# Kernel optimization log

Hardware: AMD Instinct MI355X
Metric: run time of the kernel (lower is better)

## Reference

```python
import jax, jax.numpy as jnp
import numpy as np

LAYERS, BLOCKS = 10, 3
NL = LAYERS * BLOCKS
DC, RC, SC, CLASSES, K = 128, 128, 256, 256, 2
SR = 4096  # number of output samples sliced from the end
N, L, EN = 4, 8192, 16


def _conv1x1(x, w):
    # x: [N, Cin, L], w: [Cout, Cin] -> [N, Cout, L]
    return jnp.einsum('ncl,oc->nol', x, w)


def _condition(x, enc):
    # x: [N, C, L], enc: [N, C, En], L % En == 0; tiled periodic add (faithful to the view trick)
    n, c, l = x.shape
    en = enc.shape[2]
    return (x.reshape(n, c, l // en, en) + enc[:, :, None, :]).reshape(n, c, l)


def _dilated_causal_conv(x, w, d):
    # kernel_size=2 causal dilated conv. x: [N, Cin, L], w: [Cout, Cin, 2]
    xs = jnp.pad(x, ((0, 0), (0, 0), (d, 0)))[:, :, :x.shape[2]]  # x delayed by d
    return jnp.einsum('ncl,oc->nol', xs, w[:, :, 0]) + jnp.einsum('ncl,oc->nol', x, w[:, :, 1])


def setup_inputs() -> dict:
    key = jax.random.key(0)
    ks = jax.random.split(key, 12)
    s = 0.05
    return {
        'x': jax.random.normal(ks[0], (N, CLASSES, L), jnp.float32),
        'en': jax.random.normal(ks[1], (N, CLASSES, EN), jnp.float32),
        'start1_w': jax.random.normal(ks[2], (RC, CLASSES), jnp.float32) * s,
        'start2_w': jax.random.normal(ks[3], (SC, RC), jnp.float32) * s,
        'cond_w': jax.random.normal(ks[4], (NL, 2 * DC, CLASSES), jnp.float32) * s,
        'dil_w': jax.random.normal(ks[5], (NL, 2 * DC, RC, K), jnp.float32) * s,
        'res_w': jax.random.normal(ks[6], (NL, RC, DC), jnp.float32) * s,
        'skip_w': jax.random.normal(ks[7], (NL, SC, DC), jnp.float32) * s,
        'end1_w': jax.random.normal(ks[8], (CLASSES, SC), jnp.float32) * s,
        'end1_b': jnp.zeros((CLASSES,), jnp.float32),
        'end2_w': jax.random.normal(ks[9], (CLASSES, CLASSES), jnp.float32) * s,
        'end2_b': jnp.zeros((CLASSES,), jnp.float32),
    }


def reference(x, en, start1_w, start2_w, cond_w, dil_w, res_w, skip_w,
              end1_w, end1_b, end2_w, end2_b):
    l = _conv1x1(x, start1_w)          # [N, RC, L]
    s = _conv1x1(l, start2_w)          # [N, SC, L]
    for i in range(NL):
        dil = 2 ** (i % LAYERS)
        d = _dilated_causal_conv(l, dil_w[i], dil)      # [N, 2*DC, L]
        d = _condition(d, _conv1x1(en, cond_w[i]))
        g = jax.nn.sigmoid(d[:, :DC]) * jnp.tanh(d[:, DC:])  # gated, [N, DC, L]
        l = l + _conv1x1(g, res_w[i])
        s = s + _conv1x1(g, skip_w[i])
    s = jax.nn.relu(s)
    s = _conv1x1(s, end1_w) + end1_b[None, :, None]
    s = _condition(s, _conv1x1(en, end2_w) + end2_b[None, :, None])
    s = jax.nn.relu(s)
    return s[:, :, -SR:]
```

## Files before the change

kernel.cpp:

```cpp
#include <hip/hip_runtime.h>

typedef __bf16 bf16_t;
typedef __bf16 bf16x8 __attribute__((ext_vector_type(8)));
typedef __bf16 bf16x4 __attribute__((ext_vector_type(4)));
typedef float  f32x4  __attribute__((ext_vector_type(4)));
typedef int    i32x4  __attribute__((ext_vector_type(4)));

#define PL 136
#define PX 264

__device__ __forceinline__ f32x4 mfma16(bf16x8 a, bf16x8 b, f32x4 c) {
    return __builtin_amdgcn_mfma_f32_16x16x32_bf16(a, b, c, 0, 0, 0);
}

__device__ __forceinline__ void conv_elem(const float* __restrict__ src,
                                          bf16_t* __restrict__ dst,
                                          int idx, int M, int K) {
    int MK = M * K;
    int lay = idx / MK;
    int r = idx - lay * MK;
    int j = r & 7, lane = (r >> 3) & 63, rest = r >> 9;
    int KB = K >> 5;
    int kb = rest % KB, mt = rest / KB;
    int m = mt * 16 + (lane & 15);
    int k = kb * 32 + ((lane >> 4) << 3) + j;
    dst[idx] = (bf16_t)src[(size_t)lay * MK + m * K + k];
}

__global__ void conv_all(const float* __restrict__ rw, const float* __restrict__ kw,
                         const float* __restrict__ s1w, const float* __restrict__ s2w,
                         const float* __restrict__ e1w, const float* __restrict__ dwt,
                         bf16_t* __restrict__ Ares, bf16_t* __restrict__ Askp,
                         bf16_t* __restrict__ A1, bf16_t* __restrict__ A2,
                         bf16_t* __restrict__ Ae, bf16_t* __restrict__ Adil) {
    int idx = blockIdx.x * 256 + threadIdx.x;
    if (idx < 491520) { conv_elem(rw, Ares, idx, 128, 128); return; }
    idx -= 491520;
    if (idx < 983040) { conv_elem(kw, Askp, idx, 256, 128); return; }
    idx -= 983040;
    if (idx < 32768) { conv_elem(s1w, A1, idx, 128, 256); return; }
    idx -= 32768;
    if (idx < 32768) { conv_elem(s2w, A2, idx, 256, 128); return; }
    idx -= 32768;
    if (idx < 65536) { conv_elem(e1w, Ae, idx, 256, 256); return; }
    idx -= 65536;
    if (idx < 1966080) {
        int lay = idx >> 16, r = idx & 65535;
        int j = r & 7, lane = (r >> 3) & 63, rest = r >> 9;
        int kb = rest & 7, mt = rest >> 3;
        int m = mt * 16 + (lane & 15);
        int k = kb * 32 + ((lane >> 4) << 3) + j;
        float v = (k < 128) ? dwt[(((size_t)lay * 256 + m) * 128 + k) * 2]
                            : dwt[(((size_t)lay * 256 + m) * 128 + (k - 128)) * 2 + 1];
        Adil[(size_t)lay * 65536 + r] = (bf16_t)v;
    }
}

__global__ void cond_kernel(const float* __restrict__ cond_w,
                            const float* __restrict__ end2_w,
                            const float* __restrict__ end2_b,
                            const float* __restrict__ en,
                            float* __restrict__ cond_all,
                            float* __restrict__ cond2) {
    __shared__ f32x4 en_s[1024];
    int bi = blockIdx.x;
    int i = bi >> 2, n = bi & 3, o = threadIdx.x;
    const f32x4* ep = (const f32x4*)(en + (size_t)n * 4096);
    for (int idx = threadIdx.x; idx < 1024; idx += 256) en_s[idx] = ep[idx];
    __syncthreads();
    const float* W = (i < 30) ? cond_w + ((size_t)i * 256 + o) * 256
                              : end2_w + (size_t)o * 256;
    f32x4 a0 = {0.f,0.f,0.f,0.f}, a1 = a0, a2 = a0, a3 = a0;
    for (int c = 0; c < 256; c += 4) {
        f32x4 wv = *(const f32x4*)(W + c);
        #pragma unroll
        for (int cc = 0; cc < 4; ++cc) {
            float wf = wv[cc];
            a0 += wf * en_s[(c + cc) * 4 + 0];
            a1 += wf * en_s[(c + cc) * 4 + 1];
            a2 += wf * en_s[(c + cc) * 4 + 2];
            a3 += wf * en_s[(c + cc) * 4 + 3];
        }
    }
    float bias = (i < 30) ? 0.f : end2_b[o];
    float* dst = (i < 30) ? cond_all + (((size_t)i * 4 + n) * 256 + o) * 16
                          : cond2 + ((size_t)n * 256 + o) * 16;
    f32x4* d4 = (f32x4*)dst;
    d4[0] = a0 + bias; d4[1] = a1 + bias; d4[2] = a2 + bias; d4[3] = a3 + bias;
}

__global__ __launch_bounds__(512, 4) void k_start(
    const float* __restrict__ x, bf16_t* __restrict__ la, float* __restrict__ sbuf,
    const bf16_t* __restrict__ A1, const bf16_t* __restrict__ A2, int t_base)
{
    __shared__ __align__(16) bf16_t xt[64 * PX];
    __shared__ __align__(16) bf16_t l0[64 * PL];
    int tid = threadIdx.x;
    int n = blockIdx.y, t0 = t_base + blockIdx.x * 64;
    int lane = tid & 63, w = tid >> 6, i16 = lane & 15, q = lane >> 4;
    f32x4 z = {0.f,0.f,0.f,0.f};
    {
        int t = tid & 63;
        for (int c = tid >> 6; c < 256; c += 8)
            xt[t * PX + c] = (bf16_t)x[((size_t)n * 256 + c) * 8192 + t0 + t];
    }
    __syncthreads();
    f32x4 acc[4] = {z,z,z,z};
    #pragma unroll
    for (int kb = 0; kb < 8; ++kb) {
        int koff = kb * 32 + q * 8;
        bf16x8 bf[4];
        #pragma unroll
        for (int nt = 0; nt < 4; ++nt)
            bf[nt] = *(const bf16x8*)(xt + (nt * 16 + i16) * PX + koff);
        bf16x8 af = *(const bf16x8*)(A1 + (((size_t)w * 8 + kb) * 64 + lane) * 8);
        #pragma unroll
        for (int nt = 0; nt < 4; ++nt) acc[nt] = mfma16(af, bf[nt], acc[nt]);
    }
    #pragma unroll
    for (int nt = 0; nt < 4; ++nt)
        #pragma unroll
        for (int j = 0; j < 4; ++j)
            l0[(nt * 16 + i16) * PL + w * 16 + q * 4 + j] = (bf16_t)acc[nt][j];
    __syncthreads();
    {
        int r = tid >> 4, col = (tid & 15) * 8;
        #pragma unroll
        for (int p = 0; p < 2; ++p) {
            int rr = r + p * 32;
            *(i32x4*)(la + ((size_t)n * 8192 + t0 + rr) * 128 + col) =
                *(const i32x4*)(l0 + rr * PL + col);
        }
    }
    if (t0 >= 4096) {
        f32x4 a2[2][4] = {{z,z,z,z},{z,z,z,z}};
        #pragma unroll
        for (int kb = 0; kb < 4; ++kb) {
            int koff = kb * 32 + q * 8;
            bf16x8 bf[4];
            #pragma unroll
            for (int nt = 0; nt < 4; ++nt)
                bf[nt] = *(const bf16x8*)(l0 + (nt * 16 + i16) * PL + koff);
            #pragma unroll
            for (int mt2 = 0; mt2 < 2; ++mt2) {
                bf16x8 af = *(const bf16x8*)(A2 + ((((size_t)2 * w + mt2) * 4 + kb) * 64 + lane) * 8);
                #pragma unroll
                for (int nt = 0; nt < 4; ++nt) a2[mt2][nt] = mfma16(af, bf[nt], a2[mt2][nt]);
            }
        }
        float* sp = sbuf + (size_t)n * 256 * 4096 + (t0 - 4096);
        #pragma unroll
        for (int mt2 = 0; mt2 < 2; ++mt2)
            #pragma unroll
            for (int nt = 0; nt < 4; ++nt)
                #pragma unroll
                for (int j = 0; j < 4; ++j) {
                    int o = (2 * w + mt2) * 16 + q * 4 + j;
                    sp[(size_t)o * 4096 + nt * 16 + i16] = a2[mt2][nt][j];
                }
    }
}

template<int USEG>
__global__ __launch_bounds__(512, 8) void k_layer(
    const bf16_t* __restrict__ l_in, bf16_t* __restrict__ l_out,
    float* __restrict__ sbuf, bf16_t* __restrict__ Gl,
    const bf16_t* __restrict__ Ad, const bf16_t* __restrict__ Ar,
    const bf16_t* __restrict__ Ak, const float* __restrict__ condL,
    int dil, int t_base, int do_res)
{
    __shared__ __align__(16) bf16_t sm0[32 * PL];
    __shared__ __align__(16) bf16_t sm1[32 * PL];
    __shared__ __align__(16) bf16_t sm2[32 * PL];
    int tid = threadIdx.x;
    int n = blockIdx.y, t0 = t_base + blockIdx.x * 32;
    int lane = tid & 63, w = tid >> 6, i16 = lane & 15, q = lane >> 4;
    f32x4 z = {0.f,0.f,0.f,0.f};
    const float* cond = condL + (size_t)n * 4096;
    int r = tid >> 4, col = (tid & 15) * 8;
    {
        size_t base = (size_t)n * 8192;
        *(i32x4*)(sm0 + r * PL + col) =
            *(const i32x4*)(l_in + (base + t0 + r) * 128 + col);
        int gp = t0 - dil + r;
        i32x4 v = {0, 0, 0, 0};
        if (gp >= 0) v = *(const i32x4*)(l_in + (base + gp) * 128 + col);
        *(i32x4*)(sm1 + r * PL + col) = v;
    }
    __syncthreads();

    f32x4 accs[2] = {z,z}, acct[2] = {z,z};
    const bf16x8* AdF = (const bf16x8*)Ad;
    #pragma unroll
    for (int kb = 0; kb < 8; ++kb) {
        const bf16_t* bsrc = (kb < 4) ? sm1 : sm0;
        int koff = (kb & 3) * 32 + q * 8;
        bf16x8 bf[2];
        #pragma unroll
        for (int nt = 0; nt < 2; ++nt)
            bf[nt] = *(const bf16x8*)(bsrc + (nt * 16 + i16) * PL + koff);
        bf16x8 a_s = AdF[((size_t)w * 8 + kb) * 64 + lane];
        bf16x8 a_t = AdF[((size_t)(w + 8) * 8 + kb) * 64 + lane];
        #pragma unroll
        for (int nt = 0; nt < 2; ++nt) {
            accs[nt] = mfma16(a_s, bf[nt], accs[nt]);
            acct[nt] = mfma16(a_t, bf[nt], acct[nt]);
        }
    }
    int c_base = w * 16 + q * 4;
    {
        float cv_s[4], cv_t[4];
        #pragma unroll
        for (int j = 0; j < 4; ++j) {
            cv_s[j] = cond[(c_base + j) * 16 + i16];
            cv_t[j] = cond[(c_base + j + 128) * 16 + i16];
        }
        #pragma unroll
        for (int nt = 0; nt < 2; ++nt) {
            bf16x4 g4;
            #pragma unroll
            for (int j = 0; j < 4; ++j) {
                float vlo = accs[nt][j] + cv_s[j];
                float vhi = acct[nt][j] + cv_t[j];
                float sg = 1.0f / (1.0f + __expf(-vlo));
                float th = 1.0f - 2.0f / (1.0f + __expf(2.0f * vhi));
                g4[j] = (bf16_t)(sg * th);
            }
            *(bf16x4*)(sm2 + (nt * 16 + i16) * PL + c_base) = g4;
        }
    }
    __syncthreads();

    if (USEG) {
        if (t0 >= 4096) {
            bf16_t* gd = Gl + ((size_t)n * 4096 + (t0 - 4096) + r) * 128 + col;
            *(i32x4*)gd = *(const i32x4*)(sm2 + r * PL + col);
        }
    }

    f32x4 acc2[2] = {z,z};
    const bf16x8* ArF = (const bf16x8*)Ar;
    if (do_res || !USEG) {
        int do_skip = (!USEG) && (t0 >= 4096);
        f32x4 acc3[2][2] = {{z,z},{z,z}};
        const bf16x8* AkF = (const bf16x8*)Ak;
        #pragma unroll
        for (int kb = 0; kb < 4; ++kb) {
            int koff = kb * 32 + q * 8;
            bf16x8 bf[2];
            #pragma unroll
            for (int nt = 0; nt < 2; ++nt)
                bf[nt] = *(const bf16x8*)(sm2 + (nt * 16 + i16) * PL + koff);
            if (do_res) {
                bf16x8 ar = ArF[((size_t)w * 4 + kb) * 64 + lane];
                #pragma unroll
                for (int nt = 0; nt < 2; ++nt) acc2[nt] = mfma16(ar, bf[nt], acc2[nt]);
            }
            if (do_skip) {
                #pragma unroll
                for (int mt2 = 0; mt2 < 2; ++mt2) {
                    bf16x8 ak = AkF[((size_t)(2 * w + mt2) * 4 + kb) * 64 + lane];
                    #pragma unroll
                    for (int nt = 0; nt < 2; ++nt)
                        acc3[mt2][nt] = mfma16(ak, bf[nt], acc3[mt2][nt]);
                }
            }
        }
        if (do_skip) {
            float* sp = sbuf + (size_t)n * 256 * 4096 + (t0 - 4096);
            #pragma unroll
            for (int mt2 = 0; mt2 < 2; ++mt2)
                #pragma unroll
                for (int nt = 0; nt < 2; ++nt)
                    #pragma unroll
                    for (int j = 0; j < 4; ++j) {
                        int o = (2 * w + mt2) * 16 + q * 4 + j;
                        sp[(size_t)o * 4096 + nt * 16 + i16] += acc3[mt2][nt][j];
                    }
        }
    }

    if (do_res) {
        #pragma unroll
        for (int nt = 0; nt < 2; ++nt) {
            int trow = (nt * 16 + i16) * PL;
            bf16x4 lv = *(const bf16x4*)(sm0 + trow + c_base);
            bf16x4 o4;
            #pragma unroll
            for (int j = 0; j < 4; ++j)
                o4[j] = (bf16_t)((float)lv[j] + acc2[nt][j]);
            *(bf16x4*)(sm1 + trow + c_base) = o4;
        }
        __syncthreads();
        bf16_t* dst = l_out + ((size_t)n * 8192 + t0 + r) * 128 + col;
        *(i32x4*)dst = *(const i32x4*)(sm1 + r * PL + col);
    }
}

__global__ __launch_bounds__(512, 8) void k_skip(
    const bf16_t* __restrict__ G, float* __restrict__ sbuf,
    const bf16_t* __restrict__ Askp)
{
    __shared__ __align__(16) bf16_t gbuf[32 * PL];
    int tid = threadIdx.x;
    int n = blockIdx.y, t0 = blockIdx.x * 32;
    int lane = tid & 63, w = tid >> 6, i16 = lane & 15, q = lane >> 4;
    f32x4 z = {0.f,0.f,0.f,0.f};
    f32x4 acc[2][2] = {{z,z},{z,z}};
    int r = tid >> 4, cA = (tid & 15) * 8;
    const size_t GLS = (size_t)4 * 4096 * 128;
    const bf16_t* gb = G + ((size_t)n * 4096 + t0 + r) * 128 + cA;
    i32x4 v[2];
    v[0] = *(const i32x4*)(gb);
    v[1] = *(const i32x4*)(gb + GLS);
    #pragma unroll 1
    for (int i = 0; i < 30; ++i) {
        __syncthreads();
        *(i32x4*)(gbuf + r * PL + cA) = v[i & 1];
        if (i + 2 < 30) v[i & 1] = *(const i32x4*)(gb + (size_t)(i + 2) * GLS);
        __syncthreads();
        const bf16x8* AkF = (const bf16x8*)(Askp + (size_t)i * 32768);
        #pragma unroll
        for (int kb = 0; kb < 4; ++kb) {
            int koff = kb * 32 + q * 8;
            bf16x8 ak0 = AkF[((size_t)(2 * w) * 4 + kb) * 64 + lane];
            bf16x8 ak1 = AkF[((size_t)(2 * w + 1) * 4 + kb) * 64 + lane];
            #pragma unroll
            for (int nt = 0; nt < 2; ++nt) {
                bf16x8 bf = *(const bf16x8*)(gbuf + (nt * 16 + i16) * PL + koff);
                acc[0][nt] = mfma16(ak0, bf, acc[0][nt]);
                acc[1][nt] = mfma16(ak1, bf, acc[1][nt]);
            }
        }
    }
    float* sp = sbuf + (size_t)n * 256 * 4096 + t0;
    #pragma unroll
    for (int mt2 = 0; mt2 < 2; ++mt2)
        #pragma unroll
        for (int nt = 0; nt < 2; ++nt)
            #pragma unroll
            for (int j = 0; j < 4; ++j) {
                int o = (2 * w + mt2) * 16 + q * 4 + j;
                sp[(size_t)o * 4096 + nt * 16 + i16] += acc[mt2][nt][j];
            }
}

__global__ __launch_bounds__(512) void k_end(
    const float* __restrict__ sbuf, float* __restrict__ out,
    const bf16_t* __restrict__ Ae, const float* __restrict__ cond2,
    const float* __restrict__ b1)
{
    __shared__ __align__(16) bf16_t st[64 * PX];
    __shared__ float c2[4096];
    __shared__ float b1s[256];
    int tid = threadIdx.x;
    int n = blockIdx.y, t0 = blockIdx.x * 64;
    int lane = tid & 63, w = tid >> 6, i16 = lane & 15, q = lane >> 4;
    f32x4 z = {0.f,0.f,0.f,0.f};
    {
        int t = tid & 63;
        for (int c = tid >> 6; c < 256; c += 8) {
            float v = sbuf[((size_t)n * 256 + c) * 4096 + t0 + t];
            st[t * PX + c] = (bf16_t)fmaxf(v, 0.f);
        }
        const f32x4* cc = (const f32x4*)(cond2 + (size_t)n * 4096);
        for (int idx = tid; idx < 1024; idx += 512) ((f32x4*)c2)[idx] = cc[idx];
        if (tid < 64) ((f32x4*)b1s)[tid] = ((const f32x4*)b1)[tid];
    }
    __syncthreads();
    f32x4 acc[2][4] = {{z,z,z,z},{z,z,z,z}};
    #pragma unroll
    for (int kb = 0; kb < 8; ++kb) {
        int koff = kb * 32 + q * 8;
        bf16x8 bf[4];
        #pragma unroll
        for (int nt = 0; nt < 4; ++nt)
            bf[nt] = *(const bf16x8*)(st + (nt * 16 + i16) * PX + koff);
        #pragma unroll
        for (int mt2 = 0; mt2 < 2; ++mt2) {
            bf16x8 af = *(const bf16x8*)(Ae + ((((size_t)2 * w + mt2) * 8 + kb) * 64 + lane) * 8);
            #pragma unroll
            for (int nt = 0; nt < 4; ++nt) acc[mt2][nt] = mfma16(af, bf[nt], acc[mt2][nt]);
        }
    }
    #pragma unroll
    for (int mt2 = 0; mt2 < 2; ++mt2)
        #pragma unroll
        for (int j = 0; j < 4; ++j) {
            int o = (2 * w + mt2) * 16 + q * 4 + j;
            float bb = b1s[o] + c2[o * 16 + i16];
            #pragma unroll
            for (int nt = 0; nt < 4; ++nt) {
                float v = acc[mt2][nt][j] + bb;
                out[((size_t)n * 256 + o) * 4096 + t0 + nt * 16 + i16] = fmaxf(v, 0.f);
            }
        }
}

extern "C" void kernel_launch(void* const* d_in, const int* in_sizes, int n_in,
                              void* d_out, int out_size, void* d_ws, size_t ws_size,
                              hipStream_t stream) {
    const float* x   = (const float*)d_in[0];
    const float* en  = (const float*)d_in[1];
    const float* s1w = (const float*)d_in[2];
    const float* s2w = (const float*)d_in[3];
    const float* cw  = (const float*)d_in[4];
    const float* dw  = (const float*)d_in[5];
    const float* rw  = (const float*)d_in[6];
    const float* kw  = (const float*)d_in[7];
    const float* e1w = (const float*)d_in[8];
    const float* e1b = (const float*)d_in[9];
    const float* e2w = (const float*)d_in[10];
    const float* e2b = (const float*)d_in[11];
    float* out = (float*)d_out;

    char* p = (char*)d_ws;
    auto take = [&](size_t bytes) {
        char* r = p;
        p += (bytes + 255) & ~(size_t)255;
        return r;
    };
    bf16_t* A1   = (bf16_t*)take((size_t)128 * 256 * 2);
    bf16_t* A2   = (bf16_t*)take((size_t)256 * 128 * 2);
    bf16_t* Ae   = (bf16_t*)take((size_t)256 * 256 * 2);
    bf16_t* Adil = (bf16_t*)take((size_t)30 * 65536 * 2);
    bf16_t* Ares = (bf16_t*)take((size_t)30 * 16384 * 2);
    bf16_t* Askp = (bf16_t*)take((size_t)30 * 32768 * 2);
    float*  condA= (float*)take((size_t)30 * 16384 * 4);
    float*  cond2= (float*)take((size_t)16384 * 4);
    bf16_t* la   = (bf16_t*)take((size_t)4 * 8192 * 128 * 2);
    bf16_t* lb   = (bf16_t*)take((size_t)4 * 8192 * 128 * 2);
    float*  sbuf = (float*)take((size_t)4 * 256 * 4096 * 4);
    bf16_t* G    = (bf16_t*)take((size_t)30 * 4 * 4096 * 128 * 2);
    bool useG = ((size_t)(p - (char*)d_ws) <= ws_size);

    conv_all<<<13952, 256, 0, stream>>>(rw, kw, s1w, s2w, e1w, dw,
                                        Ares, Askp, A1, A2, Ae, Adil);
    cond_kernel<<<124, 256, 0, stream>>>(cw, e2w, e2b, en, condA, cond2);

    int a[30];
    a[29] = 4096;
    for (int i = 28; i >= 0; --i) {
        int nx = a[i + 1] - (1 << ((i + 1) % 10));
        a[i] = nx < 4096 ? (nx & ~63) : 4096;
    }

    k_start<<<dim3(127, 4), 512, 0, stream>>>(x, la, sbuf, A1, A2, 64);

    bf16_t* src = la;
    bf16_t* dst = lb;
    for (int i = 0; i < 30; ++i) {
        dim3 grid((8192 - a[i]) / 32, 4);
        if (useG)
            k_layer<1><<<grid, 512, 0, stream>>>(src, dst, sbuf,
                G + (size_t)i * 4 * 4096 * 128,
                Adil + (size_t)i * 65536, Ares + (size_t)i * 16384,
                Askp + (size_t)i * 32768, condA + (size_t)i * 16384,
                1 << (i % 10), a[i], i < 29 ? 1 : 0);
        else
            k_layer<0><<<grid, 512, 0, stream>>>(src, dst, sbuf, (bf16_t*)nullptr,
                Adil + (size_t)i * 65536, Ares + (size_t)i * 16384,
                Askp + (size_t)i * 32768, condA + (size_t)i * 16384,
                1 << (i % 10), a[i], i < 29 ? 1 : 0);
        bf16_t* t = src; src = dst; dst = t;
    }
    if (useG)
        k_skip<<<dim3(128, 4), 512, 0, stream>>>(G, sbuf, Askp);
    k_end<<<dim3(64, 4), 512, 0, stream>>>(sbuf, out, Ae, cond2, e1b);
}
```

Before: 657.5 us.

## Merge prep kernels, share overlapping dilation window in smem, double-buffer skip GEMM

Folds the weight-conversion and conditioning kernels into a single launch to remove one kernel launch. In the layer kernel, small dilations (<32) now load one contiguous window of 32+dil rows, so the current and delayed tiles share overlapping rows instead of being loaded twice. The residual output is staged through a separate shared buffer with an extra barrier. The skip kernel uses two shared buffers and a 4-deep register prefetch, dropping one barrier per iteration at the cost of more registers and LDS.

```diff
diff --git a/kernel.cpp b/kernel.cpp
--- a/kernel.cpp
+++ b/kernel.cpp
@@ -27,12 +27,43 @@
     dst[idx] = (bf16_t)src[(size_t)lay * MK + m * K + k];
 }
 
-__global__ void conv_all(const float* __restrict__ rw, const float* __restrict__ kw,
-                         const float* __restrict__ s1w, const float* __restrict__ s2w,
-                         const float* __restrict__ e1w, const float* __restrict__ dwt,
-                         bf16_t* __restrict__ Ares, bf16_t* __restrict__ Askp,
-                         bf16_t* __restrict__ A1, bf16_t* __restrict__ A2,
-                         bf16_t* __restrict__ Ae, bf16_t* __restrict__ Adil) {
+__global__ void k_prep(const float* __restrict__ rw, const float* __restrict__ kw,
+                       const float* __restrict__ s1w, const float* __restrict__ s2w,
+                       const float* __restrict__ e1w, const float* __restrict__ dwt,
+                       const float* __restrict__ cond_w, const float* __restrict__ end2_w,
+                       const float* __restrict__ end2_b, const float* __restrict__ en,
+                       bf16_t* __restrict__ Ares, bf16_t* __restrict__ Askp,
+                       bf16_t* __restrict__ A1, bf16_t* __restrict__ A2,
+                       bf16_t* __restrict__ Ae, bf16_t* __restrict__ Adil,
+                       float* __restrict__ cond_all, float* __restrict__ cond2) {
+    __shared__ f32x4 en_s[1024];
+    if (blockIdx.x >= 13952) {
+        int bi = blockIdx.x - 13952;
+        int i = bi >> 2, n = bi & 3, o = threadIdx.x;
+        const f32x4* ep = (const f32x4*)(en + (size_t)n * 4096);
+        for (int idx = threadIdx.x; idx < 1024; idx += 256) en_s[idx] = ep[idx];
+        __syncthreads();
+        const float* W = (i < 30) ? cond_w + ((size_t)i * 256 + o) * 256
+                                  : end2_w + (size_t)o * 256;
+        f32x4 a0 = {0.f,0.f,0.f,0.f}, a1 = a0, a2 = a0, a3 = a0;
+        for (int c = 0; c < 256; c += 4) {
+            f32x4 wv = *(const f32x4*)(W + c);
+            #pragma unroll
+            for (int cc = 0; cc < 4; ++cc) {
+                float wf = wv[cc];
+                a0 += wf * en_s[(c + cc) * 4 + 0];
+                a1 += wf * en_s[(c + cc) * 4 + 1];
+                a2 += wf * en_s[(c + cc) * 4 + 2];
+                a3 += wf * en_s[(c + cc) * 4 + 3];
+            }
+        }
+        float bias = (i < 30) ? 0.f : end2_b[o];
+        float* dst = (i < 30) ? cond_all + (((size_t)i * 4 + n) * 256 + o) * 16
+                              : cond2 + ((size_t)n * 256 + o) * 16;
+        f32x4* d4 = (f32x4*)dst;
+        d4[0] = a0 + bias; d4[1] = a1 + bias; d4[2] = a2 + bias; d4[3] = a3 + bias;
+        return;
+    }
     int idx = blockIdx.x * 256 + threadIdx.x;
     if (idx < 491520) { conv_elem(rw, Ares, idx, 128, 128); return; }
     idx -= 491520;
@@ -44,7 +75,7 @@
     idx -= 32768;
     if (idx < 65536) { conv_elem(e1w, Ae, idx, 256, 256); return; }
     idx -= 65536;
-    if (idx < 1966080) {
+    {
         int lay = idx >> 16, r = idx & 65535;
         int j = r & 7, lane = (r >> 3) & 63, rest = r >> 9;
         int kb = rest & 7, mt = rest >> 3;
@@ -54,39 +85,6 @@
                             : dwt[(((size_t)lay * 256 + m) * 128 + (k - 128)) * 2 + 1];
         Adil[(size_t)lay * 65536 + r] = (bf16_t)v;
     }
-}
-
-__global__ void cond_kernel(const float* __restrict__ cond_w,
-                            const float* __restrict__ end2_w,
-                            const float* __restrict__ end2_b,
-                            const float* __restrict__ en,
-                            float* __restrict__ cond_all,
-                            float* __restrict__ cond2) {
-    __shared__ f32x4 en_s[1024];
-    int bi = blockIdx.x;
-    int i = bi >> 2, n = bi & 3, o = threadIdx.x;
-    const f32x4* ep = (const f32x4*)(en + (size_t)n * 4096);
-    for (int idx = threadIdx.x; idx < 1024; idx += 256) en_s[idx] = ep[idx];
-    __syncthreads();
-    const float* W = (i < 30) ? cond_w + ((size_t)i * 256 + o) * 256
-                              : end2_w + (size_t)o * 256;
-    f32x4 a0 = {0.f,0.f,0.f,0.f}, a1 = a0, a2 = a0, a3 = a0;
-    for (int c = 0; c < 256; c += 4) {
-        f32x4 wv = *(const f32x4*)(W + c);
-        #pragma unroll
-        for (int cc = 0; cc < 4; ++cc) {
-            float wf = wv[cc];
-            a0 += wf * en_s[(c + cc) * 4 + 0];
-            a1 += wf * en_s[(c + cc) * 4 + 1];
-            a2 += wf * en_s[(c + cc) * 4 + 2];
-            a3 += wf * en_s[(c + cc) * 4 + 3];
-        }
-    }
-    float bias = (i < 30) ? 0.f : end2_b[o];
-    float* dst = (i < 30) ? cond_all + (((size_t)i * 4 + n) * 256 + o) * 16
-                          : cond2 + ((size_t)n * 256 + o) * 16;
-    f32x4* d4 = (f32x4*)dst;
-    d4[0] = a0 + bias; d4[1] = a1 + bias; d4[2] = a2 + bias; d4[3] = a3 + bias;
 }
 
 __global__ __launch_bounds__(512, 4) void k_start(
@@ -169,8 +167,7 @@
     const bf16_t* __restrict__ Ak, const float* __restrict__ condL,
     int dil, int t_base, int do_res)
 {
-    __shared__ __align__(16) bf16_t sm0[32 * PL];
-    __shared__ __align__(16) bf16_t sm1[32 * PL];
+    __shared__ __align__(16) bf16_t smA[64 * PL];
     __shared__ __align__(16) bf16_t sm2[32 * PL];
     int tid = threadIdx.x;
     int n = blockIdx.y, t0 = t_base + blockIdx.x * 32;
@@ -178,14 +175,25 @@
     f32x4 z = {0.f,0.f,0.f,0.f};
     const float* cond = condL + (size_t)n * 4096;
     int r = tid >> 4, col = (tid & 15) * 8;
-    {
-        size_t base = (size_t)n * 8192;
-        *(i32x4*)(sm0 + r * PL + col) =
+    size_t base = (size_t)n * 8192;
+    const bf16_t* curp;
+    const bf16_t* delp;
+    if (dil < 32) {
+        int cnt = (32 + dil) * 16;
+        for (int idx = tid; idx < cnt; idx += 512) {
+            int rr = idx >> 4, c2 = (idx & 15) * 8;
+            *(i32x4*)(smA + rr * PL + c2) =
+                *(const i32x4*)(l_in + (base + t0 - dil + rr) * 128 + c2);
+        }
+        delp = smA; curp = smA + dil * PL;
+    } else {
+        *(i32x4*)(smA + r * PL + col) =
             *(const i32x4*)(l_in + (base + t0 + r) * 128 + col);
         int gp = t0 - dil + r;
         i32x4 v = {0, 0, 0, 0};
         if (gp >= 0) v = *(const i32x4*)(l_in + (base + gp) * 128 + col);
-        *(i32x4*)(sm1 + r * PL + col) = v;
+        *(i32x4*)(smA + (32 + r) * PL + col) = v;
+        curp = smA; delp = smA + 32 * PL;
     }
     __syncthreads();
 
@@ -193,7 +201,7 @@
     const bf16x8* AdF = (const bf16x8*)Ad;
     #pragma unroll
     for (int kb = 0; kb < 8; ++kb) {
-        const bf16_t* bsrc = (kb < 4) ? sm1 : sm0;
+        const bf16_t* bsrc = (kb < 4) ? delp : curp;
         int koff = (kb & 3) * 32 + q * 8;
         bf16x8 bf[2];
         #pragma unroll
@@ -281,19 +289,22 @@
     }
 
     if (do_res) {
+        bf16x4 o4[2];
         #pragma unroll
         for (int nt = 0; nt < 2; ++nt) {
             int trow = (nt * 16 + i16) * PL;
-            bf16x4 lv = *(const bf16x4*)(sm0 + trow + c_base);
-            bf16x4 o4;
+            bf16x4 lv = *(const bf16x4*)(curp + trow + c_base);
             #pragma unroll
             for (int j = 0; j < 4; ++j)
-                o4[j] = (bf16_t)((float)lv[j] + acc2[nt][j]);
-            *(bf16x4*)(sm1 + trow + c_base) = o4;
+                o4[nt][j] = (bf16_t)((float)lv[j] + acc2[nt][j]);
         }
         __syncthreads();
-        bf16_t* dst = l_out + ((size_t)n * 8192 + t0 + r) * 128 + col;
-        *(i32x4*)dst = *(const i32x4*)(sm1 + r * PL + col);
+        #pragma unroll
+        for (int nt = 0; nt < 2; ++nt)
+            *(bf16x4*)(sm2 + (nt * 16 + i16) * PL + c_base) = o4[nt];
+        __syncthreads();
+        bf16_t* dst = l_out + (base + t0 + r) * 128 + col;
+        *(i32x4*)dst = *(const i32x4*)(sm2 + r * PL + col);
     }
 }
 
@@ -301,7 +312,7 @@
     const bf16_t* __restrict__ G, float* __restrict__ sbuf,
     const bf16_t* __restrict__ Askp)
 {
-    __shared__ __align__(16) bf16_t gbuf[32 * PL];
+    __shared__ __align__(16) bf16_t gbuf[2][32 * PL];
     int tid = threadIdx.x;
     int n = blockIdx.y, t0 = blockIdx.x * 32;
     int lane = tid & 63, w = tid >> 6, i16 = lane & 15, q = lane >> 4;
@@ -310,16 +321,16 @@
     int r = tid >> 4, cA = (tid & 15) * 8;
     const size_t GLS = (size_t)4 * 4096 * 128;
     const bf16_t* gb = G + ((size_t)n * 4096 + t0 + r) * 128 + cA;
-    i32x4 v[2];
-    v[0] = *(const i32x4*)(gb);
-    v[1] = *(const i32x4*)(gb + GLS);
+    i32x4 v[4];
+    #pragma unroll
+    for (int d = 0; d < 4; ++d) v[d] = *(const i32x4*)(gb + (size_t)d * GLS);
     #pragma unroll 1
     for (int i = 0; i < 30; ++i) {
-        __syncthreads();
-        *(i32x4*)(gbuf + r * PL + cA) = v[i & 1];
-        if (i + 2 < 30) v[i & 1] = *(const i32x4*)(gb + (size_t)(i + 2) * GLS);
+        *(i32x4*)(gbuf[i & 1] + r * PL + cA) = v[i & 3];
+        if (i + 4 < 30) v[i & 3] = *(const i32x4*)(gb + (size_t)(i + 4) * GLS);
         __syncthreads();
         const bf16x8* AkF = (const bf16x8*)(Askp + (size_t)i * 32768);
+        const bf16_t* gB = gbuf[i & 1];
         #pragma unroll
         for (int kb = 0; kb < 4; ++kb) {
             int koff = kb * 32 + q * 8;
@@ -327,7 +338,7 @@
             bf16x8 ak1 = AkF[((size_t)(2 * w + 1) * 4 + kb) * 64 + lane];
             #pragma unroll
             for (int nt = 0; nt < 2; ++nt) {
-                bf16x8 bf = *(const bf16x8*)(gbuf + (nt * 16 + i16) * PL + koff);
+                bf16x8 bf = *(const bf16x8*)(gB + (nt * 16 + i16) * PL + koff);
                 acc[0][nt] = mfma16(ak0, bf, acc[0][nt]);
                 acc[1][nt] = mfma16(ak1, bf, acc[1][nt]);
             }
@@ -434,9 +445,9 @@
     bf16_t* G    = (bf16_t*)take((size_t)30 * 4 * 4096 * 128 * 2);
     bool useG = ((size_t)(p - (char*)d_ws) <= ws_size);
 
-    conv_all<<<13952, 256, 0, stream>>>(rw, kw, s1w, s2w, e1w, dw,
-                                        Ares, Askp, A1, A2, Ae, Adil);
-    cond_kernel<<<124, 256, 0, stream>>>(cw, e2w, e2b, en, condA, cond2);
+    k_prep<<<14076, 256, 0, stream>>>(rw, kw, s1w, s2w, e1w, dw,
+                                      cw, e2w, e2b, en,
+                                      Ares, Askp, A1, A2, Ae, Adil, condA, cond2);
 
     int a[30];
     a[29] = 4096;
```

After: 633.2 us. 3.7% less time.
